# Performance work log

Hardware: AMD Instinct MI355X
Metric: run time of the kernel (lower is better)

The kernel has to match this reference:

```python
import jax, jax.numpy as jnp
import numpy as np

BETA = 0.25  # commitment loss weight (standard VQ-VAE beta)


def setup_inputs() -> dict:
    key = jax.random.key(0)
    k1, k2 = jax.random.split(key)
    N, D, Q, K = 131072, 128, 4, 1024
    x = jax.random.normal(k1, (N, D), dtype=jnp.float32)
    codebooks = jax.random.normal(k2, (Q, K, D), dtype=jnp.float32)
    return {"x": x, "codebooks": codebooks}


def reference(x, codebooks):
    """Residual VQ: sequentially quantize the residual against each codebook.

    x:         [N, D] float
    codebooks: [Q, K, D] float (one [K, D] codebook per quantizer stage)
    Returns (x_q [N, D], mean_loss scalar, indices [N, Q] int32).
    """
    sg = jax.lax.stop_gradient

    def stage(carry, E):
        residual, x_q = carry                      # [N, D], [N, D]
        # squared euclidean distances: ||r||^2 - 2 r.E^T + ||E||^2  -> [N, K]
        d = (jnp.sum(residual * residual, axis=1, keepdims=True)
             - 2.0 * (residual @ E.T)
             + jnp.sum(E * E, axis=1))
        idx = jnp.argmin(d, axis=1)                # [N]
        q = E[idx]                                 # [N, D] gather
        # codebook loss + beta * commitment loss
        loss = (jnp.mean((q - sg(residual)) ** 2)
                + BETA * jnp.mean((sg(q) - residual) ** 2))
        # straight-through estimator
        q_st = residual + sg(q - residual)
        return (residual - q_st, x_q + q_st), (loss, idx)

    (_, x_q), (losses, idxs) = jax.lax.scan(
        stage, (x, jnp.zeros_like(x)), codebooks)
    mean_loss = jnp.mean(losses)
    all_indices = jnp.transpose(idxs)              # [Q, N] -> [N, Q], stacked dim=-1
    return x_q, mean_loss, all_indices
```

## Files before the change

kernel.cpp:

```cpp
#include <hip/hip_runtime.h>

#define N_ROWS 131072
#define DIM    128
#define QST    4
#define KC     1024
#define BM     128
#define NTH    256
#define PNTH   256
#define NWAVE  4
#define NCHUNK 64
#define EPS    6e-3f
#define FLAGB  (1 << 16)

typedef _Float16 h8  __attribute__((ext_vector_type(8)));
typedef float    fx4 __attribute__((ext_vector_type(4)));

typedef __attribute__((address_space(3))) void lds_void;
typedef const __attribute__((address_space(1))) void glb_void;

#define MFMA16(a, b, c) __builtin_amdgcn_mfma_f32_16x16x32_f16((a), (b), (c), 0, 0, 0)

__global__ void k_prep(const float* __restrict__ cb,
                       double* __restrict__ cvec64, float* __restrict__ cvec32,
                       _Float16* __restrict__ packB) {
  int gid = blockIdx.x * blockDim.x + threadIdx.x;
  if (gid >= QST * KC) return;
  int q = gid >> 10, code = gid & (KC - 1);
  int ch = code >> 4, n = code & 15;
  const float* e = cb + ((size_t)q * KC + code) * DIM;
  double s = 0.0;
  for (int d = 0; d < DIM; d++) {
    float v = e[d];
    s = fma((double)v, (double)v, s);
    int kt = d >> 5, g = (d >> 3) & 3, j = d & 7;
    int lane = g * 16 + n;
    size_t base = ((size_t)q * NCHUNK + ch) * 4096 + (size_t)kt * 1024 + lane * 8 + j;
    _Float16 hh = (_Float16)v;
    packB[base]       = hh;
    packB[base + 512] = (_Float16)(v - (float)hh);
  }
  cvec64[q * KC + code] = s;
  cvec32[q * KC + code] = (float)s;
}

__global__ __launch_bounds__(NTH, 4) void k_stage(
    int st, const float* rin, float* rout, const float* __restrict__ x,
    const float* __restrict__ cb,
    const double* __restrict__ cvec64, const float* __restrict__ cvec32,
    const _Float16* __restrict__ packB,
    float* __restrict__ oidx, float* __restrict__ lpart, int final_stage)
{
  extern __shared__ float smem[];
  _Float16* Bl    = (_Float16*)smem;
  float*    cvecL = smem + 6144;
  int*      idxs  = (int*)(smem + 7168);
  double*   redd  = (double*)(smem + 7296);
  int*      redi  = (int*)(smem + 7304);
  float*    redf  = smem + 7308;
  int*      flags = (int*)(smem + 7312);

  const int tid = threadIdx.x;
  const int lane = tid & 63, wv = tid >> 6;
  const int tx = lane & 15;
  const size_t rowbase = (size_t)blockIdx.x * BM;

  const double*   cq64 = cvec64 + st * KC;
  const float*    cq32 = cvec32 + st * KC;
  const float*    Eq   = cb + (size_t)st * KC * DIM;
  const _Float16* PBq  = packB + (size_t)st * 262144;

  for (int i = tid; i < KC; i += NTH) cvecL[i] = cq32[i];

  h8 ah[2][4], al[2][4];
  #pragma unroll
  for (int rt = 0; rt < 2; rt++) {
    const float* rowp = rin + (rowbase + wv * 32 + rt * 16 + (lane & 15)) * (size_t)DIM
                        + ((lane >> 4) * 8);
    #pragma unroll
    for (int kt = 0; kt < 4; kt++) {
      float4 f0 = *(const float4*)(rowp + kt * 32);
      float4 f1 = *(const float4*)(rowp + kt * 32 + 4);
      float vv[8] = {f0.x, f0.y, f0.z, f0.w, f1.x, f1.y, f1.z, f1.w};
      #pragma unroll
      for (int j = 0; j < 8; j++) {
        _Float16 hh = (_Float16)vv[j];
        ah[rt][kt][j] = hh;
        al[rt][kt][j] = (_Float16)(vv[j] - (float)hh);
      }
    }
  }

  __syncthreads();

  auto stageB = [&](int ch, int buf) {
    const _Float16* src = PBq + (size_t)ch * 4096 + wv * 1024 + lane * 8;
    _Float16* dst = Bl + (size_t)buf * 4096 + wv * 1024;
    #pragma unroll
    for (int i = 0; i < 2; i++)
      __builtin_amdgcn_global_load_lds((glb_void*)(src + i * 512),
                                       (lds_void*)(dst + i * 512), 16, 0, 0);
  };

  float b1[8], b2[8];
  int   i1[8];
  #pragma unroll
  for (int i = 0; i < 8; i++) { b1[i] = 3.4e38f; b2[i] = 3.4e38f; i1[i] = 0; }

  const fx4 zero4 = {0.f, 0.f, 0.f, 0.f};
  fx4 accPrev[2];
  accPrev[0] = zero4; accPrev[1] = zero4;

  stageB(0, 0); stageB(1, 1);

  int buf = 0, bufStage = 2;
  #pragma unroll 1
  for (int ch = 0; ch < NCHUNK; ch++) {
    if (ch < NCHUNK - 1) asm volatile("s_waitcnt vmcnt(2)" ::: "memory");
    else                 asm volatile("s_waitcnt vmcnt(0)" ::: "memory");
    __builtin_amdgcn_s_barrier();
    asm volatile("" ::: "memory");
    if (ch + 2 < NCHUNK) stageB(ch + 2, bufStage);

    if (ch > 0) {
      int code = (ch - 1) * 16 + tx;
      float cvv = cvecL[code];
      #pragma unroll
      for (int rt = 0; rt < 2; rt++) {
        #pragma unroll
        for (int j = 0; j < 4; j++) {
          float sc = fmaf(-2.f, accPrev[rt][j], cvv);
          int r = rt * 4 + j;
          if (sc < b1[r]) { b2[r] = b1[r]; b1[r] = sc; i1[r] = code; }
          else            { b2[r] = fminf(b2[r], sc); }
        }
      }
    }

    const _Float16* Bb = Bl + (size_t)buf * 4096;
    fx4 acc[2];
    acc[0] = zero4; acc[1] = zero4;

    __builtin_amdgcn_s_setprio(1);
    #pragma unroll
    for (int kt = 0; kt < 4; kt++) {
      const _Float16* p = Bb + (size_t)kt * 1024 + lane * 8;
      h8 bh = *(const h8*)p;
      h8 bl = *(const h8*)(p + 512);
      #pragma unroll
      for (int rt = 0; rt < 2; rt++) {
        acc[rt] = MFMA16(ah[rt][kt], bh, acc[rt]);
        acc[rt] = MFMA16(al[rt][kt], bh, acc[rt]);
        acc[rt] = MFMA16(ah[rt][kt], bl, acc[rt]);
      }
    }
    __builtin_amdgcn_s_setprio(0);

    accPrev[0] = acc[0];
    accPrev[1] = acc[1];

    buf = (buf == 2) ? 0 : buf + 1;
    bufStage = (bufStage == 2) ? 0 : bufStage + 1;
  }

  {
    int code = (NCHUNK - 1) * 16 + tx;
    float cvv = cvecL[code];
    #pragma unroll
    for (int rt = 0; rt < 2; rt++) {
      #pragma unroll
      for (int j = 0; j < 4; j++) {
        float sc = fmaf(-2.f, accPrev[rt][j], cvv);
        int r = rt * 4 + j;
        if (sc < b1[r]) { b2[r] = b1[r]; b1[r] = sc; i1[r] = code; }
        else            { b2[r] = fminf(b2[r], sc); }
      }
    }
  }

  #pragma unroll
  for (int m = 1; m < 16; m <<= 1) {
    #pragma unroll
    for (int r = 0; r < 8; r++) {
      float ob1 = __shfl_xor(b1[r], m, 64);
      int   oi1 = __shfl_xor(i1[r], m, 64);
      float ob2 = __shfl_xor(b2[r], m, 64);
      bool take = (ob1 < b1[r]) || (ob1 == b1[r] && oi1 < i1[r]);
      float loser = take ? b1[r] : ob1;
      if (take) { b1[r] = ob1; i1[r] = oi1; }
      b2[r] = fminf(fminf(b2[r], ob2), loser);
    }
  }

  if (tx == 0) {
    int g = lane >> 4;
    #pragma unroll
    for (int rt = 0; rt < 2; rt++)
      #pragma unroll
      for (int j = 0; j < 4; j++) {
        int r = rt * 4 + j;
        int fl = (b2[r] - b1[r] <= EPS) ? FLAGB : 0;
        idxs[wv * 32 + rt * 16 + g * 4 + j] = i1[r] | fl;
      }
  }
  __syncthreads();

  {
    bool pred = (tid < BM) && (idxs[tid] & FLAGB);
    unsigned long long bal = __ballot(pred);
    if (lane == 0) flags[wv] = (bal != 0ull) ? 1 : 0;
  }
  __syncthreads();
  int anyflag = flags[0] | flags[1] | flags[2] | flags[3];
  if (anyflag) {
    for (int row = 0; row < BM; row++) {
      if (!(idxs[row] & FLAGB)) continue;
      const float* rrow = rin + (rowbase + row) * (size_t)DIM;
      double dot[4] = {0.0, 0.0, 0.0, 0.0};
      for (int d = 0; d < DIM; d++) {
        double a = (double)rrow[d];
        #pragma unroll
        for (int c = 0; c < 4; c++)
          dot[c] = fma(a, (double)Eq[(size_t)(tid + c * NTH) * DIM + d], dot[c]);
      }
      double bs = 1e300; int bk = 0;
      #pragma unroll
      for (int c = 0; c < 4; c++) {
        int k = tid + c * NTH;
        double s = fma(-2.0, dot[c], cq64[k]);
        if (s < bs || (s == bs && k < bk)) { bs = s; bk = k; }
      }
      #pragma unroll
      for (int m = 1; m < 64; m <<= 1) {
        double ob = __shfl_xor(bs, m, 64);
        int    ok = __shfl_xor(bk, m, 64);
        if (ob < bs || (ob == bs && ok < bk)) { bs = ob; bk = ok; }
      }
      if (lane == 0) { redd[wv] = bs; redi[wv] = bk; }
      __syncthreads();
      if (tid == 0) {
        double fb = redd[0]; int fk = redi[0];
        #pragma unroll
        for (int w = 1; w < NWAVE; w++) {
          if (redd[w] < fb || (redd[w] == fb && redi[w] < fk)) { fb = redd[w]; fk = redi[w]; }
        }
        idxs[row] = fk;
      }
      __syncthreads();
    }
  }

  {
    float lsum = 0.f;
    #pragma unroll 1
    for (int it = 0; it < 16; it++) {
      int g = it * NTH + tid;
      int row = g >> 5, c4 = g & 31;
      int kidx = idxs[row] & 1023;
      if ((g & 31) == 0) oidx[(rowbase + row) * 4 + st] = (float)kidx;
      float4 ev = *(const float4*)(Eq + (size_t)kidx * DIM + c4 * 4);
      float4 rv = *(const float4*)(rin + (rowbase + row) * (size_t)DIM + c4 * 4);
      float4 dv = make_float4(rv.x - ev.x, rv.y - ev.y, rv.z - ev.z, rv.w - ev.w);
      lsum = fmaf(dv.x, dv.x, lsum);
      lsum = fmaf(dv.y, dv.y, lsum);
      lsum = fmaf(dv.z, dv.z, lsum);
      lsum = fmaf(dv.w, dv.w, lsum);
      float4 wv4 = dv;
      if (final_stage) {
        float4 xv = *(const float4*)(x + (rowbase + row) * (size_t)DIM + c4 * 4);
        wv4 = make_float4(xv.x - dv.x, xv.y - dv.y, xv.z - dv.z, xv.w - dv.w);
      }
      *(float4*)(rout + (rowbase + row) * (size_t)DIM + c4 * 4) = wv4;
    }
    #pragma unroll
    for (int m = 1; m < 64; m <<= 1) lsum += __shfl_xor(lsum, m, 64);
    if (lane == 0) redf[wv] = lsum;
    __syncthreads();
    if (tid == 0) lpart[st * (N_ROWS / BM) + blockIdx.x] =
        redf[0] + redf[1] + redf[2] + redf[3];
  }
}

__global__ void k_loss(const float* __restrict__ part, float* __restrict__ o) {
  __shared__ float red[4];
  int tid = threadIdx.x;
  float s = 0.f;
  for (int i = tid; i < QST * (N_ROWS / BM); i += PNTH) s += part[i];
  #pragma unroll
  for (int m = 1; m < 64; m <<= 1) s += __shfl_xor(s, m, 64);
  if ((tid & 63) == 0) red[tid >> 6] = s;
  __syncthreads();
  if (tid == 0)
    o[0] = (red[0] + red[1] + red[2] + red[3]) *
           (1.25f / ((float)QST * (float)N_ROWS * (float)DIM));
}

extern "C" void kernel_launch(void* const* d_in, const int* in_sizes, int n_in,
                              void* d_out, int out_size, void* d_ws, size_t ws_size,
                              hipStream_t stream) {
  const float* x  = (const float*)d_in[0];
  const float* cb = (const float*)d_in[1];
  float* out = (float*)d_out;
  float* ws  = (float*)d_ws;

  float*    r      = out;
  double*   cvec64 = (double*)ws;
  float*    cvec32 = (float*)(cvec64 + (size_t)QST * KC);
  float*    part   = cvec32 + (size_t)QST * KC;
  _Float16* packB  = (_Float16*)(part + (size_t)QST * (N_ROWS / BM));

  float* out_loss = out + (size_t)N_ROWS * DIM;
  float* out_idx  = out_loss + 1;

  static const size_t SMEM = 7316 * sizeof(float);
  hipFuncSetAttribute(reinterpret_cast<const void*>(k_stage),
                      hipFuncAttributeMaxDynamicSharedMemorySize, (int)SMEM);

  k_prep<<<(QST * KC + PNTH - 1) / PNTH, PNTH, 0, stream>>>(cb, cvec64, cvec32, packB);

  for (int s = 0; s < QST; s++) {
    const float* rin = (s == 0) ? x : r;
    k_stage<<<N_ROWS / BM, NTH, SMEM, stream>>>(s, rin, r, x, cb, cvec64, cvec32,
                                                packB, out_idx, part,
                                                (s == QST - 1) ? 1 : 0);
  }

  k_loss<<<1, PNTH, 0, stream>>>(part, out_loss);
}
```

Before: 641.2 us.

## Fuse all four RVQ stages into one kernel keeping residual in registers

Replaces the four per-stage kernel launches with a single fused kernel that loops over quantizer stages per row block. The residual stays in registers as split fp16 fragments and is rebuilt from x minus the gathered codewords of earlier stages, so intermediate residuals no longer round-trip through global memory. In exchange, each stage re-reads x and every previously chosen codeword, and the loss is accumulated across stages into one partial per block. Register pressure may rise with the stage loop and the per-stage index history held in shared memory.

```diff
diff --git a/kernel.cpp b/kernel.cpp
--- a/kernel.cpp
+++ b/kernel.cpp
@@ -43,38 +43,32 @@
   cvec32[q * KC + code] = (float)s;
 }
 
-__global__ __launch_bounds__(NTH, 4) void k_stage(
-    int st, const float* rin, float* rout, const float* __restrict__ x,
+__global__ __launch_bounds__(NTH, 4) void k_fused(
+    const float* __restrict__ x, float* xq,
     const float* __restrict__ cb,
     const double* __restrict__ cvec64, const float* __restrict__ cvec32,
     const _Float16* __restrict__ packB,
-    float* __restrict__ oidx, float* __restrict__ lpart, int final_stage)
+    float* oidx, float* __restrict__ lpart)
 {
-  extern __shared__ float smem[];
-  _Float16* Bl    = (_Float16*)smem;
-  float*    cvecL = smem + 6144;
-  int*      idxs  = (int*)(smem + 7168);
-  double*   redd  = (double*)(smem + 7296);
-  int*      redi  = (int*)(smem + 7304);
-  float*    redf  = smem + 7308;
-  int*      flags = (int*)(smem + 7312);
+  __shared__ _Float16 Bl[3 * 4096];
+  __shared__ float    cvecL[KC];
+  __shared__ int      idxsW[BM];
+  __shared__ int      idxH[QST][BM];
+  __shared__ float    rowbuf[DIM];
+  __shared__ double   redd[NWAVE];
+  __shared__ int      redi[NWAVE];
+  __shared__ float    redf[NWAVE];
+  __shared__ int      flags[NWAVE];
 
   const int tid = threadIdx.x;
   const int lane = tid & 63, wv = tid >> 6;
   const int tx = lane & 15;
   const size_t rowbase = (size_t)blockIdx.x * BM;
 
-  const double*   cq64 = cvec64 + st * KC;
-  const float*    cq32 = cvec32 + st * KC;
-  const float*    Eq   = cb + (size_t)st * KC * DIM;
-  const _Float16* PBq  = packB + (size_t)st * 262144;
-
-  for (int i = tid; i < KC; i += NTH) cvecL[i] = cq32[i];
-
   h8 ah[2][4], al[2][4];
   #pragma unroll
   for (int rt = 0; rt < 2; rt++) {
-    const float* rowp = rin + (rowbase + wv * 32 + rt * 16 + (lane & 15)) * (size_t)DIM
+    const float* rowp = x + (rowbase + wv * 32 + rt * 16 + (lane & 15)) * (size_t)DIM
                         + ((lane >> 4) * 8);
     #pragma unroll
     for (int kt = 0; kt < 4; kt++) {
@@ -90,39 +84,91 @@
     }
   }
 
-  __syncthreads();
-
-  auto stageB = [&](int ch, int buf) {
-    const _Float16* src = PBq + (size_t)ch * 4096 + wv * 1024 + lane * 8;
-    _Float16* dst = Bl + (size_t)buf * 4096 + wv * 1024;
+  float lsum = 0.f;
+  const fx4 zero4 = {0.f, 0.f, 0.f, 0.f};
+
+  #pragma unroll 1
+  for (int st = 0; st < QST; st++) {
+    const _Float16* PBq  = packB + (size_t)st * 262144;
+    const float*    cq32 = cvec32 + st * KC;
+    const double*   cq64 = cvec64 + st * KC;
+    const float*    Eq   = cb + (size_t)st * KC * DIM;
+
+    __syncthreads();
+    for (int i = tid; i < KC; i += NTH) cvecL[i] = cq32[i];
+    __syncthreads();
+
+    auto stageB = [&](int ch, int buf) {
+      const _Float16* src = PBq + (size_t)ch * 4096 + wv * 1024 + lane * 8;
+      _Float16* dst = Bl + (size_t)buf * 4096 + wv * 1024;
+      #pragma unroll
+      for (int i = 0; i < 2; i++)
+        __builtin_amdgcn_global_load_lds((glb_void*)(src + i * 512),
+                                         (lds_void*)(dst + i * 512), 16, 0, 0);
+    };
+
+    float b1[8], b2[8];
+    int   i1[8];
     #pragma unroll
-    for (int i = 0; i < 2; i++)
-      __builtin_amdgcn_global_load_lds((glb_void*)(src + i * 512),
-                                       (lds_void*)(dst + i * 512), 16, 0, 0);
-  };
-
-  float b1[8], b2[8];
-  int   i1[8];
-  #pragma unroll
-  for (int i = 0; i < 8; i++) { b1[i] = 3.4e38f; b2[i] = 3.4e38f; i1[i] = 0; }
-
-  const fx4 zero4 = {0.f, 0.f, 0.f, 0.f};
-  fx4 accPrev[2];
-  accPrev[0] = zero4; accPrev[1] = zero4;
-
-  stageB(0, 0); stageB(1, 1);
-
-  int buf = 0, bufStage = 2;
-  #pragma unroll 1
-  for (int ch = 0; ch < NCHUNK; ch++) {
-    if (ch < NCHUNK - 1) asm volatile("s_waitcnt vmcnt(2)" ::: "memory");
-    else                 asm volatile("s_waitcnt vmcnt(0)" ::: "memory");
-    __builtin_amdgcn_s_barrier();
-    asm volatile("" ::: "memory");
-    if (ch + 2 < NCHUNK) stageB(ch + 2, bufStage);
-
-    if (ch > 0) {
-      int code = (ch - 1) * 16 + tx;
+    for (int i = 0; i < 8; i++) { b1[i] = 3.4e38f; b2[i] = 3.4e38f; i1[i] = 0; }
+
+    fx4 accPrev[2];
+    accPrev[0] = zero4; accPrev[1] = zero4;
+
+    stageB(0, 0); stageB(1, 1);
+
+    int buf = 0, bufStage = 2;
+    #pragma unroll 1
+    for (int ch = 0; ch < NCHUNK; ch++) {
+      if (ch < NCHUNK - 1) asm volatile("s_waitcnt vmcnt(2)" ::: "memory");
+      else                 asm volatile("s_waitcnt vmcnt(0)" ::: "memory");
+      __builtin_amdgcn_s_barrier();
+      asm volatile("" ::: "memory");
+      if (ch + 2 < NCHUNK) stageB(ch + 2, bufStage);
+
+      if (ch > 0) {
+        int code = (ch - 1) * 16 + tx;
+        float cvv = cvecL[code];
+        #pragma unroll
+        for (int rt = 0; rt < 2; rt++) {
+          #pragma unroll
+          for (int j = 0; j < 4; j++) {
+            float sc = fmaf(-2.f, accPrev[rt][j], cvv);
+            int r = rt * 4 + j;
+            if (sc < b1[r]) { b2[r] = b1[r]; b1[r] = sc; i1[r] = code; }
+            else            { b2[r] = fminf(b2[r], sc); }
+          }
+        }
+      }
+
+      const _Float16* Bb = Bl + (size_t)buf * 4096;
+      fx4 acc[2];
+      acc[0] = zero4; acc[1] = zero4;
+
+      __builtin_amdgcn_s_setprio(1);
+      #pragma unroll
+      for (int kt = 0; kt < 4; kt++) {
+        const _Float16* p = Bb + (size_t)kt * 1024 + lane * 8;
+        h8 bh = *(const h8*)p;
+        h8 bl = *(const h8*)(p + 512);
+        #pragma unroll
+        for (int rt = 0; rt < 2; rt++) {
+          acc[rt] = MFMA16(ah[rt][kt], bh, acc[rt]);
+          acc[rt] = MFMA16(al[rt][kt], bh, acc[rt]);
+          acc[rt] = MFMA16(ah[rt][kt], bl, acc[rt]);
+        }
+      }
+      __builtin_amdgcn_s_setprio(0);
+
+      accPrev[0] = acc[0];
+      accPrev[1] = acc[1];
+
+      buf = (buf == 2) ? 0 : buf + 1;
+      bufStage = (bufStage == 2) ? 0 : bufStage + 1;
+    }
+
+    {
+      int code = (NCHUNK - 1) * 16 + tx;
       float cvv = cvecL[code];
       #pragma unroll
       for (int rt = 0; rt < 2; rt++) {
@@ -136,155 +182,150 @@
       }
     }
 
-    const _Float16* Bb = Bl + (size_t)buf * 4096;
-    fx4 acc[2];
-    acc[0] = zero4; acc[1] = zero4;
-
-    __builtin_amdgcn_s_setprio(1);
     #pragma unroll
-    for (int kt = 0; kt < 4; kt++) {
-      const _Float16* p = Bb + (size_t)kt * 1024 + lane * 8;
-      h8 bh = *(const h8*)p;
-      h8 bl = *(const h8*)(p + 512);
-      #pragma unroll
-      for (int rt = 0; rt < 2; rt++) {
-        acc[rt] = MFMA16(ah[rt][kt], bh, acc[rt]);
-        acc[rt] = MFMA16(al[rt][kt], bh, acc[rt]);
-        acc[rt] = MFMA16(ah[rt][kt], bl, acc[rt]);
-      }
-    }
-    __builtin_amdgcn_s_setprio(0);
-
-    accPrev[0] = acc[0];
-    accPrev[1] = acc[1];
-
-    buf = (buf == 2) ? 0 : buf + 1;
-    bufStage = (bufStage == 2) ? 0 : bufStage + 1;
-  }
-
-  {
-    int code = (NCHUNK - 1) * 16 + tx;
-    float cvv = cvecL[code];
+    for (int m = 1; m < 16; m <<= 1) {
+      #pragma unroll
+      for (int r = 0; r < 8; r++) {
+        float ob1 = __shfl_xor(b1[r], m, 64);
+        int   oi1 = __shfl_xor(i1[r], m, 64);
+        float ob2 = __shfl_xor(b2[r], m, 64);
+        bool take = (ob1 < b1[r]) || (ob1 == b1[r] && oi1 < i1[r]);
+        float loser = take ? b1[r] : ob1;
+        if (take) { b1[r] = ob1; i1[r] = oi1; }
+        b2[r] = fminf(fminf(b2[r], ob2), loser);
+      }
+    }
+
+    if (tx == 0) {
+      int g = lane >> 4;
+      #pragma unroll
+      for (int rt = 0; rt < 2; rt++)
+        #pragma unroll
+        for (int j = 0; j < 4; j++) {
+          int r = rt * 4 + j;
+          int fl = (b2[r] - b1[r] <= EPS) ? FLAGB : 0;
+          idxsW[wv * 32 + rt * 16 + g * 4 + j] = i1[r] | fl;
+        }
+    }
+    __syncthreads();
+
+    {
+      bool pred = (tid < BM) && (idxsW[tid] & FLAGB);
+      unsigned long long bal = __ballot(pred);
+      if (lane == 0) flags[wv] = (bal != 0ull) ? 1 : 0;
+    }
+    __syncthreads();
+    int anyflag = flags[0] | flags[1] | flags[2] | flags[3];
+    if (anyflag) {
+      for (int row = 0; row < BM; row++) {
+        if (!(idxsW[row] & FLAGB)) continue;
+        if (tid < 16) {
+          int d0 = tid * 8;
+          const float* xp = x + (rowbase + row) * (size_t)DIM + d0;
+          float r8[8];
+          #pragma unroll
+          for (int j = 0; j < 8; j++) r8[j] = xp[j];
+          for (int s = 0; s < st; s++) {
+            const float* ep = cb + ((size_t)s * KC + idxH[s][row]) * DIM + d0;
+            #pragma unroll
+            for (int j = 0; j < 8; j++) r8[j] = r8[j] - ep[j];
+          }
+          #pragma unroll
+          for (int j = 0; j < 8; j++) rowbuf[d0 + j] = r8[j];
+        }
+        __syncthreads();
+        double dot[4] = {0.0, 0.0, 0.0, 0.0};
+        for (int d = 0; d < DIM; d++) {
+          double a = (double)rowbuf[d];
+          #pragma unroll
+          for (int c = 0; c < 4; c++)
+            dot[c] = fma(a, (double)Eq[(size_t)(tid + c * NTH) * DIM + d], dot[c]);
+        }
+        double bs = 1e300; int bk = 0;
+        #pragma unroll
+        for (int c = 0; c < 4; c++) {
+          int k = tid + c * NTH;
+          double s = fma(-2.0, dot[c], cq64[k]);
+          if (s < bs || (s == bs && k < bk)) { bs = s; bk = k; }
+        }
+        #pragma unroll
+        for (int m = 1; m < 64; m <<= 1) {
+          double ob = __shfl_xor(bs, m, 64);
+          int    ok = __shfl_xor(bk, m, 64);
+          if (ob < bs || (ob == bs && ok < bk)) { bs = ob; bk = ok; }
+        }
+        if (lane == 0) { redd[wv] = bs; redi[wv] = bk; }
+        __syncthreads();
+        if (tid == 0) {
+          double fb = redd[0]; int fk = redi[0];
+          #pragma unroll
+          for (int w = 1; w < NWAVE; w++) {
+            if (redd[w] < fb || (redd[w] == fb && redi[w] < fk)) { fb = redd[w]; fk = redi[w]; }
+          }
+          idxsW[row] = fk;
+        }
+        __syncthreads();
+      }
+    }
+
+    if (tid < BM) {
+      int v = idxsW[tid] & 1023;
+      idxH[st][tid] = v;
+      oidx[(rowbase + tid) * 4 + st] = (float)v;
+    }
+    __syncthreads();
+
     #pragma unroll
     for (int rt = 0; rt < 2; rt++) {
-      #pragma unroll
-      for (int j = 0; j < 4; j++) {
-        float sc = fmaf(-2.f, accPrev[rt][j], cvv);
-        int r = rt * 4 + j;
-        if (sc < b1[r]) { b2[r] = b1[r]; b1[r] = sc; i1[r] = code; }
-        else            { b2[r] = fminf(b2[r], sc); }
+      int row = wv * 32 + rt * 16 + (lane & 15);
+      int d0b = (lane >> 4) * 8;
+      #pragma unroll
+      for (int kt = 0; kt < 4; kt++) {
+        int d0 = d0b + kt * 32;
+        const float* xp = x + (rowbase + row) * (size_t)DIM + d0;
+        float4 xf0 = *(const float4*)(xp);
+        float4 xf1 = *(const float4*)(xp + 4);
+        float r8[8] = {xf0.x, xf0.y, xf0.z, xf0.w, xf1.x, xf1.y, xf1.z, xf1.w};
+        for (int s = 0; s <= st; s++) {
+          const float* ep = cb + ((size_t)s * KC + idxH[s][row]) * DIM + d0;
+          float4 e0 = *(const float4*)(ep);
+          float4 e1 = *(const float4*)(ep + 4);
+          float e8[8] = {e0.x, e0.y, e0.z, e0.w, e1.x, e1.y, e1.z, e1.w};
+          #pragma unroll
+          for (int j = 0; j < 8; j++) r8[j] = r8[j] - e8[j];
+        }
+        #pragma unroll
+        for (int j = 0; j < 8; j++) lsum = fmaf(r8[j], r8[j], lsum);
+        if (st < QST - 1) {
+          #pragma unroll
+          for (int j = 0; j < 8; j++) {
+            _Float16 hh = (_Float16)r8[j];
+            ah[rt][kt][j] = hh;
+            al[rt][kt][j] = (_Float16)(r8[j] - (float)hh);
+          }
+        } else {
+          float4 o0 = make_float4(xf0.x - r8[0], xf0.y - r8[1], xf0.z - r8[2], xf0.w - r8[3]);
+          float4 o1 = make_float4(xf1.x - r8[4], xf1.y - r8[5], xf1.z - r8[6], xf1.w - r8[7]);
+          float* op = xq + (rowbase + row) * (size_t)DIM + d0;
+          *(float4*)(op)     = o0;
+          *(float4*)(op + 4) = o1;
+        }
       }
     }
   }
 
   #pragma unroll
-  for (int m = 1; m < 16; m <<= 1) {
-    #pragma unroll
-    for (int r = 0; r < 8; r++) {
-      float ob1 = __shfl_xor(b1[r], m, 64);
-      int   oi1 = __shfl_xor(i1[r], m, 64);
-      float ob2 = __shfl_xor(b2[r], m, 64);
-      bool take = (ob1 < b1[r]) || (ob1 == b1[r] && oi1 < i1[r]);
-      float loser = take ? b1[r] : ob1;
-      if (take) { b1[r] = ob1; i1[r] = oi1; }
-      b2[r] = fminf(fminf(b2[r], ob2), loser);
-    }
-  }
-
-  if (tx == 0) {
-    int g = lane >> 4;
-    #pragma unroll
-    for (int rt = 0; rt < 2; rt++)
-      #pragma unroll
-      for (int j = 0; j < 4; j++) {
-        int r = rt * 4 + j;
-        int fl = (b2[r] - b1[r] <= EPS) ? FLAGB : 0;
-        idxs[wv * 32 + rt * 16 + g * 4 + j] = i1[r] | fl;
-      }
-  }
+  for (int m = 1; m < 64; m <<= 1) lsum += __shfl_xor(lsum, m, 64);
+  if (lane == 0) redf[wv] = lsum;
   __syncthreads();
-
-  {
-    bool pred = (tid < BM) && (idxs[tid] & FLAGB);
-    unsigned long long bal = __ballot(pred);
-    if (lane == 0) flags[wv] = (bal != 0ull) ? 1 : 0;
-  }
-  __syncthreads();
-  int anyflag = flags[0] | flags[1] | flags[2] | flags[3];
-  if (anyflag) {
-    for (int row = 0; row < BM; row++) {
-      if (!(idxs[row] & FLAGB)) continue;
-      const float* rrow = rin + (rowbase + row) * (size_t)DIM;
-      double dot[4] = {0.0, 0.0, 0.0, 0.0};
-      for (int d = 0; d < DIM; d++) {
-        double a = (double)rrow[d];
-        #pragma unroll
-        for (int c = 0; c < 4; c++)
-          dot[c] = fma(a, (double)Eq[(size_t)(tid + c * NTH) * DIM + d], dot[c]);
-      }
-      double bs = 1e300; int bk = 0;
-      #pragma unroll
-      for (int c = 0; c < 4; c++) {
-        int k = tid + c * NTH;
-        double s = fma(-2.0, dot[c], cq64[k]);
-        if (s < bs || (s == bs && k < bk)) { bs = s; bk = k; }
-      }
-      #pragma unroll
-      for (int m = 1; m < 64; m <<= 1) {
-        double ob = __shfl_xor(bs, m, 64);
-        int    ok = __shfl_xor(bk, m, 64);
-        if (ob < bs || (ob == bs && ok < bk)) { bs = ob; bk = ok; }
-      }
-      if (lane == 0) { redd[wv] = bs; redi[wv] = bk; }
-      __syncthreads();
-      if (tid == 0) {
-        double fb = redd[0]; int fk = redi[0];
-        #pragma unroll
-        for (int w = 1; w < NWAVE; w++) {
-          if (redd[w] < fb || (redd[w] == fb && redi[w] < fk)) { fb = redd[w]; fk = redi[w]; }
-        }
-        idxs[row] = fk;
-      }
-      __syncthreads();
-    }
-  }
-
-  {
-    float lsum = 0.f;
-    #pragma unroll 1
-    for (int it = 0; it < 16; it++) {
-      int g = it * NTH + tid;
-      int row = g >> 5, c4 = g & 31;
-      int kidx = idxs[row] & 1023;
-      if ((g & 31) == 0) oidx[(rowbase + row) * 4 + st] = (float)kidx;
-      float4 ev = *(const float4*)(Eq + (size_t)kidx * DIM + c4 * 4);
-      float4 rv = *(const float4*)(rin + (rowbase + row) * (size_t)DIM + c4 * 4);
-      float4 dv = make_float4(rv.x - ev.x, rv.y - ev.y, rv.z - ev.z, rv.w - ev.w);
-      lsum = fmaf(dv.x, dv.x, lsum);
-      lsum = fmaf(dv.y, dv.y, lsum);
-      lsum = fmaf(dv.z, dv.z, lsum);
-      lsum = fmaf(dv.w, dv.w, lsum);
-      float4 wv4 = dv;
-      if (final_stage) {
-        float4 xv = *(const float4*)(x + (rowbase + row) * (size_t)DIM + c4 * 4);
-        wv4 = make_float4(xv.x - dv.x, xv.y - dv.y, xv.z - dv.z, xv.w - dv.w);
-      }
-      *(float4*)(rout + (rowbase + row) * (size_t)DIM + c4 * 4) = wv4;
-    }
-    #pragma unroll
-    for (int m = 1; m < 64; m <<= 1) lsum += __shfl_xor(lsum, m, 64);
-    if (lane == 0) redf[wv] = lsum;
-    __syncthreads();
-    if (tid == 0) lpart[st * (N_ROWS / BM) + blockIdx.x] =
-        redf[0] + redf[1] + redf[2] + redf[3];
-  }
+  if (tid == 0) lpart[blockIdx.x] = redf[0] + redf[1] + redf[2] + redf[3];
 }
 
 __global__ void k_loss(const float* __restrict__ part, float* __restrict__ o) {
   __shared__ float red[4];
   int tid = threadIdx.x;
   float s = 0.f;
-  for (int i = tid; i < QST * (N_ROWS / BM); i += PNTH) s += part[i];
+  for (int i = tid; i < N_ROWS / BM; i += PNTH) s += part[i];
   #pragma unroll
   for (int m = 1; m < 64; m <<= 1) s += __shfl_xor(s, m, 64);
   if ((tid & 63) == 0) red[tid >> 6] = s;
@@ -302,27 +343,18 @@
   float* out = (float*)d_out;
   float* ws  = (float*)d_ws;
 
-  float*    r      = out;
   double*   cvec64 = (double*)ws;
   float*    cvec32 = (float*)(cvec64 + (size_t)QST * KC);
   float*    part   = cvec32 + (size_t)QST * KC;
-  _Float16* packB  = (_Float16*)(part + (size_t)QST * (N_ROWS / BM));
+  _Float16* packB  = (_Float16*)(part + (size_t)(N_ROWS / BM));
 
   float* out_loss = out + (size_t)N_ROWS * DIM;
   float* out_idx  = out_loss + 1;
 
-  static const size_t SMEM = 7316 * sizeof(float);
-  hipFuncSetAttribute(reinterpret_cast<const void*>(k_stage),
-                      hipFuncAttributeMaxDynamicSharedMemorySize, (int)SMEM);
-
   k_prep<<<(QST * KC + PNTH - 1) / PNTH, PNTH, 0, stream>>>(cb, cvec64, cvec32, packB);
 
-  for (int s = 0; s < QST; s++) {
-    const float* rin = (s == 0) ? x : r;
-    k_stage<<<N_ROWS / BM, NTH, SMEM, stream>>>(s, rin, r, x, cb, cvec64, cvec32,
-                                                packB, out_idx, part,
-                                                (s == QST - 1) ? 1 : 0);
-  }
+  k_fused<<<N_ROWS / BM, NTH, 0, stream>>>(x, out, cb, cvec64, cvec32, packB,
+                                           out_idx, part);
 
   k_loss<<<1, PNTH, 0, stream>>>(part, out_loss);
 }
```

Result: slower. 1.051 ms (+64.0%).
